# Optimization experiments

Hardware: AMD Instinct MI355X
Metric: run time of the kernel (lower is better)

The kernel has to match this reference:

```python
import jax, jax.numpy as jnp
import numpy as np

N_NODES = 50000
N_EDGES = 800000
H_DIM = 128
HIDDEN = 256


def _glorot(key, shape):
    fan_in, fan_out = shape[1], shape[0]
    lim = np.sqrt(6.0 / (fan_in + fan_out)).astype(np.float32)
    return jax.random.uniform(key, shape, jnp.float32, -lim, lim)


def setup_inputs() -> dict:
    key = jax.random.key(0)
    ks = jax.random.split(key, 12)
    h = jax.random.normal(ks[0], (N_NODES, H_DIM), jnp.float32)
    coord_diff = jax.random.normal(ks[1], (N_EDGES, 3), jnp.float32)
    row = jax.random.randint(ks[2], (N_EDGES,), 0, N_NODES, jnp.int64)
    col = jax.random.randint(ks[3], (N_EDGES,), 0, N_NODES, jnp.int64)
    # edge MLP: Linear(2*H+1 -> HIDDEN), SiLU, Linear(HIDDEN -> HIDDEN), SiLU
    We1 = _glorot(ks[4], (HIDDEN, 2 * H_DIM + 1))
    be1 = jnp.zeros((HIDDEN,), jnp.float32)
    We2 = _glorot(ks[5], (HIDDEN, HIDDEN))
    be2 = jnp.zeros((HIDDEN,), jnp.float32)
    # node MLP: Linear(HIDDEN + H -> HIDDEN), SiLU, Linear(HIDDEN -> H)
    Wn1 = _glorot(ks[6], (HIDDEN, HIDDEN + H_DIM))
    bn1 = jnp.zeros((HIDDEN,), jnp.float32)
    Wn2 = _glorot(ks[7], (H_DIM, HIDDEN))
    bn2 = jnp.zeros((H_DIM,), jnp.float32)
    return {"h": h, "coord_diff": coord_diff, "row": row, "col": col,
            "We1": We1, "be1": be1, "We2": We2, "be2": be2,
            "Wn1": Wn1, "bn1": bn1, "Wn2": Wn2, "bn2": bn2}


def reference(h, coord_diff, row, col, We1, be1, We2, be2, Wn1, bn1, Wn2, bn2):
    # radial: squared edge length, [E, 1]
    radial = jnp.sum(coord_diff ** 2, axis=1, keepdims=True)
    # edge model: gather endpoints, concat, 2-layer SiLU MLP
    e_in = jnp.concatenate([h[row], h[col], radial], axis=1)  # [E, 2H+1]
    m = jax.nn.silu(e_in @ We1.T + be1)                        # [E, HIDDEN]
    m = jax.nn.silu(m @ We2.T + be2)                           # [E, HIDDEN]
    # node model: scatter-add messages to source node `row`
    agg = jax.ops.segment_sum(m, row, num_segments=h.shape[0])  # [N, HIDDEN]
    n_in = jnp.concatenate([h, agg], axis=1)                    # [N, HIDDEN+H]
    out = jax.nn.silu(n_in @ Wn1.T + bn1) @ Wn2.T + bn2         # [N, H]
    return out
```

## Files before the change

kernel.cpp:

```cpp
#include <hip/hip_runtime.h>
#include <cstdint>
#include <cstddef>

#define E_EDGES 800000
#define N_NODES 50000
#define HDIM 128
#define HID 256
#define ME 64
#define NB 64
#define NTILES 196

typedef __attribute__((ext_vector_type(8))) short short8;
typedef __attribute__((ext_vector_type(4))) float f32x4;

__device__ __forceinline__ float silu(float y) {
    return y * __builtin_amdgcn_rcpf(1.0f + __expf(-y));
}

__device__ __forceinline__ short f2bfn(float f) {
    __bf16 b = (__bf16)f;
    return __builtin_bit_cast(short, b);
}
__device__ __forceinline__ float bf2f(short s) {
    return __uint_as_float(((unsigned int)(unsigned short)s) << 16);
}

#define PREP_H    6250
#define PREP_AGG  (PREP_H + 12500)
#define PREP_HIST (PREP_AGG + 3125)
#define PREP_WAB  (PREP_HIST + 320)
#define PREP_WRF  (PREP_WAB + 1)
#define PREP_WE2  (PREP_WRF + 288)
#define PREP_WN1  (PREP_WE2 + 416)
#define PREP_WN2  (PREP_WN1 + 144)
__global__ void prep_kernel(const float* __restrict__ h, short* __restrict__ hbf,
                            float* __restrict__ agg,
                            const int* __restrict__ row, int* __restrict__ cnt,
                            const float* __restrict__ We1, const float* __restrict__ be1,
                            short* __restrict__ Wab, float* __restrict__ wrf,
                            const float* __restrict__ We2, const float* __restrict__ be2,
                            short* __restrict__ Wb2,
                            const float* __restrict__ Wn1, const float* __restrict__ bn1,
                            short* __restrict__ Wbn1,
                            const float* __restrict__ Wn2, const float* __restrict__ bn2,
                            short* __restrict__ Wbn2) {
    const int b = blockIdx.x, t = threadIdx.x;
    if (b < PREP_H) {
        int i = b * 256 + t;
        float4 v = ((const float4*)h)[i];
        short4 s;
        s.x = f2bfn(v.x); s.y = f2bfn(v.y); s.z = f2bfn(v.z); s.w = f2bfn(v.w);
        ((short4*)hbf)[i] = s;
    } else if (b < PREP_AGG) {
        int i = (b - PREP_H) * 256 + t;
        ((float4*)agg)[i] = make_float4(0.f, 0.f, 0.f, 0.f);
    } else if (b < PREP_HIST) {
        int e = (b - PREP_AGG) * 256 + t;
        if (e < E_EDGES) atomicAdd(&cnt[row[e]], 1);
    } else if (b < PREP_WAB) {
        int idx = (b - PREP_HIST) * 256 + t;
        int c = idx / 160, k = idx - c * 160;
        short v = 0;
        if (c < 256) {
            if (k < 128)       v = f2bfn(We1[c * 257 + k]);
            else if (k == 128) v = f2bfn(be1[c]);
        } else {
            if (k < 128)       v = f2bfn(We1[(c - 256) * 257 + 128 + k]);
        }
        Wab[idx] = v;
    } else if (b < PREP_WRF) {
        wrf[t] = We1[t * 257 + 256];
    } else if (b < PREP_WE2) {
        int idx = (b - PREP_WRF) * 256 + t;
        int c = idx / 288, k = idx - c * 288;
        short v = 0;
        if (k < 256)       v = f2bfn(We2[c * 256 + k]);
        else if (k == 256) v = f2bfn(be2[c]);
        Wb2[idx] = v;
    } else if (b < PREP_WN1) {
        int idx = (b - PREP_WE2) * 256 + t;
        int c = idx / 416, k = idx - c * 416;
        short v = 0;
        if (k < 384)       v = f2bfn(Wn1[c * 384 + k]);
        else if (k == 384) v = f2bfn(bn1[c]);
        Wbn1[idx] = v;
    } else {
        int idx = (b - PREP_WN1) * 256 + t;
        int c = idx / 288, k = idx - c * 288;
        short v = 0;
        if (k < 256)       v = f2bfn(Wn2[c * 256 + k]);
        else if (k == 256) v = f2bfn(bn2[c]);
        Wbn2[idx] = v;
    }
}

__global__ void scanA_kernel(const int* __restrict__ cnt, int* __restrict__ incl,
                             int* __restrict__ tsum) {
    const int b = blockIdx.x, t = threadIdx.x;
    const int i = b * 256 + t;
    const int lane = t & 63, wv = t >> 6;
    int v = (i < N_NODES) ? cnt[i] : 0;
    int s = v;
#pragma unroll
    for (int off = 1; off < 64; off <<= 1) {
        int u = __shfl_up(s, off, 64);
        if (lane >= off) s += u;
    }
    __shared__ int wsum[4];
    if (lane == 63) wsum[wv] = s;
    __syncthreads();
    int pre = 0;
#pragma unroll
    for (int j = 0; j < 3; ++j) if (wv > j) pre += wsum[j];
    s += pre;
    if (i < N_NODES) incl[i] = s;
    if (t == 255) tsum[b] = s;
}

__global__ void scanB_kernel(const int* __restrict__ tsum, int* __restrict__ toff) {
    const int t = threadIdx.x;
    const int lane = t & 63, wv = t >> 6;
    int v = (t < NTILES) ? tsum[t] : 0;
    int s = v;
#pragma unroll
    for (int off = 1; off < 64; off <<= 1) {
        int u = __shfl_up(s, off, 64);
        if (lane >= off) s += u;
    }
    __shared__ int wsum[4];
    if (lane == 63) wsum[wv] = s;
    __syncthreads();
    int pre = 0;
#pragma unroll
    for (int j = 0; j < 3; ++j) if (wv > j) pre += wsum[j];
    s += pre;
    if (t < NTILES) toff[t] = s - v;
}

__global__ void scanC_kernel(const int* __restrict__ cnt, int* __restrict__ cursor,
                             const int* __restrict__ toff) {
    const int b = blockIdx.x, t = threadIdx.x;
    const int i = b * 256 + t;
    if (i < N_NODES) {
        cursor[i] = cursor[i] - cnt[i] + toff[b];
    }
}

__global__ void fill_kernel(const int* __restrict__ row, int* __restrict__ cursor,
                            int* __restrict__ eidx) {
    int e = blockIdx.x * 256 + threadIdx.x;
    if (e < E_EDGES) {
        int pos = atomicAdd(&cursor[row[e]], 1);
        eidx[pos] = e;
    }
}

__global__ __launch_bounds__(256, 4) void hab_kernel(
    const short* __restrict__ hbf, const short* __restrict__ Wab,
    short* __restrict__ hab)
{
    __shared__ __align__(16) short shH[NB * 128];
    __shared__ __align__(16) short shTh[NB * 32];

    const int t = threadIdx.x;
    const int tile = blockIdx.x >> 1;
    const int half = blockIdx.x & 1;
    const int n0 = tile * NB;

    {
        const int n = t >> 2, q = t & 3;
        int gn = n0 + n;
        if (gn >= N_NODES) gn = N_NODES - 1;
        const short8* hp = (const short8*)(hbf + (size_t)gn * HDIM + q * 32);
#pragma unroll
        for (int c = 0; c < 4; ++c) {
            short8 v = hp[c];
            int chunk = q * 4 + c;
            *(short8*)&shH[n * 128 + ((chunk ^ (n & 7)) << 3)] = v;
        }
        short8 z = {0, 0, 0, 0, 0, 0, 0, 0};
        if (q == 0) z[0] = (short)0x3F80;
        *(short8*)&shTh[n * 32 + ((q ^ (n & 3)) << 3)] = z;
    }
    __syncthreads();

    const int l = t & 63, w = t >> 6;
    const int l15 = l & 15, lq = l >> 4;

    f32x4 acc[4][4];
#pragma unroll
    for (int i = 0; i < 4; ++i)
#pragma unroll
        for (int j = 0; j < 4; ++j) acc[i][j] = (f32x4){0.f, 0.f, 0.f, 0.f};

#pragma unroll
    for (int ks = 0; ks < 5; ++ks) {
        short8 a[4], b[4];
#pragma unroll
        for (int et = 0; et < 4; ++et) {
            int r = et * 16 + l15;
            if (ks < 4) {
                int chunk = ks * 4 + lq;
                a[et] = *(const short8*)&shH[r * 128 + ((chunk ^ (r & 7)) << 3)];
            } else {
                a[et] = *(const short8*)&shTh[r * 32 + ((lq ^ (r & 3)) << 3)];
            }
        }
#pragma unroll
        for (int ct = 0; ct < 4; ++ct) {
            int cc = half * 256 + w * 64 + ct * 16 + l15;
            b[ct] = *(const short8*)&Wab[cc * 160 + ks * 32 + lq * 8];
        }
#pragma unroll
        for (int et = 0; et < 4; ++et)
#pragma unroll
            for (int ct = 0; ct < 4; ++ct)
                acc[et][ct] = __builtin_amdgcn_mfma_f32_16x16x32_bf16(
                    a[et], b[ct], acc[et][ct], 0, 0, 0);
    }

#pragma unroll
    for (int et = 0; et < 4; ++et) {
#pragma unroll
        for (int ct = 0; ct < 4; ++ct) {
            int cc = half * 256 + w * 64 + ct * 16 + l15;
#pragma unroll
            for (int r4 = 0; r4 < 4; ++r4) {
                int gn = n0 + et * 16 + lq * 4 + r4;
                if (gn < N_NODES)
                    hab[(size_t)gn * 512 + cc] = f2bfn(acc[et][ct][r4]);
            }
        }
    }
}

__global__ __launch_bounds__(256, 4) void edge_kernel(
    const short* __restrict__ hab, const float* __restrict__ coord,
    const int* __restrict__ row, const int* __restrict__ col,
    const int* __restrict__ eidx, const float* __restrict__ wrf,
    const short* __restrict__ Wb2, float* __restrict__ agg)
{
    __shared__ __align__(16) short shPool[ME * 256 + ME * 32];
    __shared__ int sr[ME];
    short* shA = shPool;
    short* shT = shPool + ME * 256;

    const int t = threadIdx.x;
    const int nwg = E_EDGES / ME;
    const int qq = nwg >> 3, rr = nwg & 7;
    const int xcd = blockIdx.x & 7, bi = blockIdx.x >> 3;
    const int wg = (xcd < rr ? xcd * (qq + 1) : rr * (qq + 1) + (xcd - rr) * qq) + bi;
    const int e0 = wg * ME;

    {
        const int e = t >> 2, q = t & 3;
        const int eo = eidx[e0 + e];
        const int rsrc = row[eo];
        const int csrc = col[eo];
        float cx = coord[3 * eo + 0];
        float cy = coord[3 * eo + 1];
        float cz = coord[3 * eo + 2];
        float radial = cx * cx + cy * cy + cz * cz;
        const short8* Ap = (const short8*)(hab + (size_t)rsrc * 512 + q * 64);
        const short8* Bp = (const short8*)(hab + (size_t)csrc * 512 + 256 + q * 64);
        const f32x4* Wp = (const f32x4*)(wrf + q * 64);
#pragma unroll
        for (int j = 0; j < 8; ++j) {
            short8 av = Ap[j];
            short8 bv = Bp[j];
            f32x4 w0 = Wp[2 * j], w1 = Wp[2 * j + 1];
            short8 o;
#pragma unroll
            for (int u = 0; u < 4; ++u) {
                float y = bf2f(av[u]) + bf2f(bv[u]) + radial * w0[u];
                o[u] = f2bfn(silu(y));
            }
#pragma unroll
            for (int u = 0; u < 4; ++u) {
                float y = bf2f(av[4 + u]) + bf2f(bv[4 + u]) + radial * w1[u];
                o[4 + u] = f2bfn(silu(y));
            }
            int chunk = q * 8 + j;
            *(short8*)&shA[e * 256 + ((chunk ^ (e & 7)) << 3)] = o;
        }
        short8 z = {0, 0, 0, 0, 0, 0, 0, 0};
        if (q == 0) {
            z[0] = (short)0x3F80;
            sr[e] = rsrc;
        }
        *(short8*)&shT[e * 32 + ((q ^ (e & 3)) << 3)] = z;
    }
    __syncthreads();

    const int l = t & 63, w = t >> 6;
    const int l15 = l & 15, lq = l >> 4;

    f32x4 acc[4][4];
#pragma unroll
    for (int i = 0; i < 4; ++i)
#pragma unroll
        for (int j = 0; j < 4; ++j) acc[i][j] = (f32x4){0.f, 0.f, 0.f, 0.f};
#pragma unroll
    for (int ks = 0; ks < 8; ++ks) {
        short8 a[4], b[4];
#pragma unroll
        for (int et = 0; et < 4; ++et) {
            int r = et * 16 + l15;
            int chunk = ks * 4 + lq;
            a[et] = *(const short8*)&shA[r * 256 + ((chunk ^ (r & 7)) << 3)];
        }
#pragma unroll
        for (int ct = 0; ct < 4; ++ct) {
            int cc = w * 64 + ct * 16 + l15;
            b[ct] = *(const short8*)&Wb2[cc * 288 + ks * 32 + lq * 8];
        }
        __builtin_amdgcn_s_setprio(1);
#pragma unroll
        for (int et = 0; et < 4; ++et)
#pragma unroll
            for (int ct = 0; ct < 4; ++ct)
                acc[et][ct] = __builtin_amdgcn_mfma_f32_16x16x32_bf16(
                    a[et], b[ct], acc[et][ct], 0, 0, 0);
        __builtin_amdgcn_s_setprio(0);
    }
    {
        short8 a[4], b[4];
#pragma unroll
        for (int et = 0; et < 4; ++et) {
            int r = et * 16 + l15;
            a[et] = *(const short8*)&shT[r * 32 + ((lq ^ (r & 3)) << 3)];
        }
#pragma unroll
        for (int ct = 0; ct < 4; ++ct) {
            int cc = w * 64 + ct * 16 + l15;
            b[ct] = *(const short8*)&Wb2[cc * 288 + 256 + lq * 8];
        }
        __builtin_amdgcn_s_setprio(1);
#pragma unroll
        for (int et = 0; et < 4; ++et)
#pragma unroll
            for (int ct = 0; ct < 4; ++ct)
                acc[et][ct] = __builtin_amdgcn_mfma_f32_16x16x32_bf16(
                    a[et], b[ct], acc[et][ct], 0, 0, 0);
        __builtin_amdgcn_s_setprio(0);
    }
    __syncthreads();

    {
#pragma unroll
        for (int ct = 0; ct < 4; ++ct) {
#pragma unroll
            for (int et = 0; et < 4; ++et) {
                int kc = w * 64 + ct * 16 + l15;
                int er0 = et * 16 + lq * 4;
                short4 s;
                s.x = f2bfn(silu(acc[et][ct][0]));
                s.y = f2bfn(silu(acc[et][ct][1]));
                s.z = f2bfn(silu(acc[et][ct][2]));
                s.w = f2bfn(silu(acc[et][ct][3]));
                *(short4*)&shPool[kc * 68 + er0] = s;
            }
        }
    }
    __syncthreads();

    {
        const int cc = t;
        const short* myrow = &shPool[cc * 68];
        float accum = 0.f;
        int cur = __builtin_amdgcn_readfirstlane(sr[0]);
        for (int eb = 0; eb < ME; eb += 4) {
            short4 v4 = *(const short4*)&myrow[eb];
            short vj[4] = {v4.x, v4.y, v4.z, v4.w};
#pragma unroll
            for (int j = 0; j < 4; ++j) {
                float v = bf2f(vj[j]);
                int r = __builtin_amdgcn_readfirstlane(sr[eb + j]);
                if (r != cur) {
                    atomicAdd(&agg[(size_t)cur * HID + cc], accum);
                    accum = v;
                    cur = r;
                } else {
                    accum += v;
                }
            }
        }
        atomicAdd(&agg[(size_t)cur * HID + cc], accum);
    }
}

__global__ __launch_bounds__(256, 3) void node_kernel(
    const short* __restrict__ hbf, const float* __restrict__ agg,
    const short* __restrict__ Wbn1, const short* __restrict__ Wbn2,
    float* __restrict__ out)
{
    __shared__ __align__(16) short pool[NB * 384];
    __shared__ __align__(16) short shTn[NB * 32];
    short* shH  = pool;
    short* shAg = pool + NB * 128;
    short* shM  = pool;

    const int t  = threadIdx.x;
    const int n0 = blockIdx.x * NB;

    {
        const int n = t >> 2, q = t & 3;
        int gn = n0 + n;
        if (gn >= N_NODES) gn = N_NODES - 1;
        const short8* hp = (const short8*)(hbf + (size_t)gn * HDIM + q * 32);
#pragma unroll
        for (int c = 0; c < 4; ++c) {
            short8 v = hp[c];
            int chunk = q * 4 + c;
            int sw = chunk ^ (n & 7);
            *(short8*)&shH[n * 128 + sw * 8] = v;
        }
        const float4* ap = (const float4*)(agg + (size_t)gn * HID + q * 64);
#pragma unroll
        for (int i = 0; i < 8; ++i) {
            float4 u0 = ap[2 * i], u1 = ap[2 * i + 1];
            short8 s;
            s[0] = f2bfn(u0.x); s[1] = f2bfn(u0.y); s[2] = f2bfn(u0.z); s[3] = f2bfn(u0.w);
            s[4] = f2bfn(u1.x); s[5] = f2bfn(u1.y); s[6] = f2bfn(u1.z); s[7] = f2bfn(u1.w);
            int chunk = q * 8 + i;
            int sw2 = chunk ^ (n & 7);
            *(short8*)&shAg[n * 256 + sw2 * 8] = s;
        }
        short8 z = {0, 0, 0, 0, 0, 0, 0, 0};
        if (q == 0) z[0] = (short)0x3F80;
        *(short8*)&shTn[n * 32 + ((q ^ (n & 3)) << 3)] = z;
    }
    __syncthreads();

    const int l = t & 63, w = t >> 6;
    const int l15 = l & 15, lq = l >> 4;

    f32x4 acc[4][4];
#pragma unroll
    for (int i = 0; i < 4; ++i)
#pragma unroll
        for (int j = 0; j < 4; ++j) acc[i][j] = (f32x4){0.f, 0.f, 0.f, 0.f};
#pragma unroll
    for (int ks = 0; ks < 12; ++ks) {
        short8 a[4], b[4];
#pragma unroll
        for (int et = 0; et < 4; ++et) {
            int r = et * 16 + l15;
            if (ks < 4) {
                int chunk = ks * 4 + lq;
                a[et] = *(const short8*)&shH[r * 128 + ((chunk ^ (r & 7)) << 3)];
            } else {
                int chunk = (ks - 4) * 4 + lq;
                a[et] = *(const short8*)&shAg[r * 256 + ((chunk ^ (r & 7)) << 3)];
            }
        }
#pragma unroll
        for (int ct = 0; ct < 4; ++ct) {
            int cc = w * 64 + ct * 16 + l15;
            b[ct] = *(const short8*)&Wbn1[cc * 416 + ks * 32 + lq * 8];
        }
#pragma unroll
        for (int et = 0; et < 4; ++et)
#pragma unroll
            for (int ct = 0; ct < 4; ++ct)
                acc[et][ct] = __builtin_amdgcn_mfma_f32_16x16x32_bf16(
                    a[et], b[ct], acc[et][ct], 0, 0, 0);
    }
    {
        short8 a[4], b[4];
#pragma unroll
        for (int et = 0; et < 4; ++et) {
            int r = et * 16 + l15;
            a[et] = *(const short8*)&shTn[r * 32 + ((lq ^ (r & 3)) << 3)];
        }
#pragma unroll
        for (int ct = 0; ct < 4; ++ct) {
            int cc = w * 64 + ct * 16 + l15;
            b[ct] = *(const short8*)&Wbn1[cc * 416 + 384 + lq * 8];
        }
#pragma unroll
        for (int et = 0; et < 4; ++et)
#pragma unroll
            for (int ct = 0; ct < 4; ++ct)
                acc[et][ct] = __builtin_amdgcn_mfma_f32_16x16x32_bf16(
                    a[et], b[ct], acc[et][ct], 0, 0, 0);
    }
    __syncthreads();

    {
#pragma unroll
        for (int et = 0; et < 4; ++et) {
#pragma unroll
            for (int rp = 0; rp < 2; ++rp) {
                int er0 = et * 16 + lq * 4 + rp * 2;
#pragma unroll
                for (int ct = 0; ct < 4; ++ct) {
                    int kc = w * 64 + ct * 16 + l15;
                    float y0 = silu(acc[et][ct][rp * 2]);
                    float y1 = silu(acc[et][ct][rp * 2 + 1]);
                    int khi = kc >> 3, klo = kc & 7;
                    shM[er0 * 256 + ((khi ^ (er0 & 7)) << 3) + klo] = f2bfn(y0);
                    shM[(er0 + 1) * 256 + ((khi ^ ((er0 + 1) & 7)) << 3) + klo] = f2bfn(y1);
                }
            }
        }
    }
    __syncthreads();

    f32x4 acc2[4][2];
#pragma unroll
    for (int i = 0; i < 4; ++i)
#pragma unroll
        for (int j = 0; j < 2; ++j) acc2[i][j] = (f32x4){0.f, 0.f, 0.f, 0.f};
#pragma unroll
    for (int ks = 0; ks < 8; ++ks) {
        short8 a[4], b2[2];
#pragma unroll
        for (int et = 0; et < 4; ++et) {
            int r = et * 16 + l15;
            int chunk = ks * 4 + lq;
            a[et] = *(const short8*)&shM[r * 256 + ((chunk ^ (r & 7)) << 3)];
        }
#pragma unroll
        for (int ct = 0; ct < 2; ++ct) {
            int cc = w * 32 + ct * 16 + l15;
            b2[ct] = *(const short8*)&Wbn2[cc * 288 + ks * 32 + lq * 8];
        }
#pragma unroll
        for (int et = 0; et < 4; ++et)
#pragma unroll
            for (int ct = 0; ct < 2; ++ct)
                acc2[et][ct] = __builtin_amdgcn_mfma_f32_16x16x32_bf16(
                    a[et], b2[ct], acc2[et][ct], 0, 0, 0);
    }
    {
        short8 a[4], b2[2];
#pragma unroll
        for (int et = 0; et < 4; ++et) {
            int r = et * 16 + l15;
            a[et] = *(const short8*)&shTn[r * 32 + ((lq ^ (r & 3)) << 3)];
        }
#pragma unroll
        for (int ct = 0; ct < 2; ++ct) {
            int cc = w * 32 + ct * 16 + l15;
            b2[ct] = *(const short8*)&Wbn2[cc * 288 + 256 + lq * 8];
        }
#pragma unroll
        for (int et = 0; et < 4; ++et)
#pragma unroll
            for (int ct = 0; ct < 2; ++ct)
                acc2[et][ct] = __builtin_amdgcn_mfma_f32_16x16x32_bf16(
                    a[et], b2[ct], acc2[et][ct], 0, 0, 0);
    }

#pragma unroll
    for (int et = 0; et < 4; ++et) {
#pragma unroll
        for (int ct = 0; ct < 2; ++ct) {
            int cc = w * 32 + ct * 16 + l15;
#pragma unroll
            for (int r4 = 0; r4 < 4; ++r4) {
                int gn = n0 + et * 16 + lq * 4 + r4;
                if (gn < N_NODES)
                    out[(size_t)gn * HDIM + cc] = acc2[et][ct][r4];
            }
        }
    }
}

extern "C" void kernel_launch(void* const* d_in, const int* in_sizes, int n_in,
                              void* d_out, int out_size, void* d_ws, size_t ws_size,
                              hipStream_t stream) {
    const float* h   = (const float*)d_in[0];
    const float* cd  = (const float*)d_in[1];
    const int*   row = (const int*)d_in[2];
    const int*   col = (const int*)d_in[3];
    const float* We1 = (const float*)d_in[4];
    const float* be1 = (const float*)d_in[5];
    const float* We2 = (const float*)d_in[6];
    const float* be2 = (const float*)d_in[7];
    const float* Wn1 = (const float*)d_in[8];
    const float* bn1 = (const float*)d_in[9];
    const float* Wn2 = (const float*)d_in[10];
    const float* bn2 = (const float*)d_in[11];
    float* out = (float*)d_out;

    short* Wab  = (short*)d_ws;
    short* Wb2  = Wab + 512 * 160;
    short* Wbn1 = Wb2 + 256 * 288;
    short* Wbn2 = Wbn1 + 256 * 416;
    float* wrf  = (float*)(Wbn2 + 128 * 288);
    short* hbf  = (short*)(wrf + 256);
    short* hab  = hbf + (size_t)N_NODES * HDIM;
    float* agg  = (float*)(hab + (size_t)N_NODES * 512);
    int*   cnt    = (int*)(agg + (size_t)N_NODES * HID);
    int*   cursor = cnt + N_NODES;
    int*   eidx   = cursor + N_NODES;
    int*   tsum   = eidx + E_EDGES;
    int*   toff   = tsum + 256;

    hipMemsetAsync(cnt, 0, N_NODES * sizeof(int), stream);

    prep_kernel<<<PREP_WN2, 256, 0, stream>>>(h, hbf, agg, row, cnt,
                                              We1, be1, Wab, wrf,
                                              We2, be2, Wb2,
                                              Wn1, bn1, Wbn1, Wn2, bn2, Wbn2);

    hab_kernel<<<((N_NODES + NB - 1) / NB) * 2, 256, 0, stream>>>(hbf, Wab, hab);

    scanA_kernel<<<NTILES, 256, 0, stream>>>(cnt, cursor, tsum);
    scanB_kernel<<<1, 256, 0, stream>>>(tsum, toff);
    scanC_kernel<<<NTILES, 256, 0, stream>>>(cnt, cursor, toff);
    fill_kernel<<<(E_EDGES + 255) / 256, 256, 0, stream>>>(row, cursor, eidx);

    edge_kernel<<<E_EDGES / ME, 256, 0, stream>>>(hab, cd, row, col, eidx, wrf,
                                                  Wb2, agg);
    node_kernel<<<(N_NODES + NB - 1) / NB, 256, 0, stream>>>(hbf, agg, Wbn1, Wbn2, out);
}
```

Measured before the change: 492.4 us.

## Gather endpoint features into LDS with async global_load_lds in edge kernel

The edge kernel's gather of the row and column endpoint feature rows now goes straight into shared memory through asynchronous global-to-LDS 16-byte loads. Each wave broadcasts row and column indices by shuffle and lays the data out with an XOR swizzle. The SiLU pre-activation then reads both halves from LDS, with radial values and radial weights staged in shared memory, and writes results in place. The aim is to cut register traffic and improve latency hiding on the random gathers. In exchange LDS use roughly doubles, so launch bounds drop from 4 to 2 blocks per CU, which lowers occupancy.

```diff
diff --git a/kernel.cpp b/kernel.cpp
--- a/kernel.cpp
+++ b/kernel.cpp
@@ -23,6 +23,12 @@
 }
 __device__ __forceinline__ float bf2f(short s) {
     return __uint_as_float(((unsigned int)(unsigned short)s) << 16);
+}
+
+__device__ __forceinline__ void async16(void* lds, const void* g) {
+    __builtin_amdgcn_global_load_lds(
+        (const __attribute__((address_space(1))) unsigned int*)g,
+        (__attribute__((address_space(3))) unsigned int*)lds, 16, 0, 0);
 }
 
 #define PREP_H    6250
@@ -234,16 +240,17 @@
     }
 }
 
-__global__ __launch_bounds__(256, 4) void edge_kernel(
+__global__ __launch_bounds__(256, 2) void edge_kernel(
     const short* __restrict__ hab, const float* __restrict__ coord,
     const int* __restrict__ row, const int* __restrict__ col,
     const int* __restrict__ eidx, const float* __restrict__ wrf,
     const short* __restrict__ Wb2, float* __restrict__ agg)
 {
-    __shared__ __align__(16) short shPool[ME * 256 + ME * 32];
-    __shared__ int sr[ME];
-    short* shA = shPool;
-    short* shT = shPool + ME * 256;
+    __shared__ __align__(16) short shPool[ME * 512];
+    __shared__ __align__(16) short shT[ME * 32];
+    __shared__ int   sr[ME];
+    __shared__ float srad[ME];
+    __shared__ __align__(16) float shWr[HID];
 
     const int t = threadIdx.x;
     const int nwg = E_EDGES / ME;
@@ -252,48 +259,71 @@
     const int wg = (xcd < rr ? xcd * (qq + 1) : rr * (qq + 1) + (xcd - rr) * qq) + bi;
     const int e0 = wg * ME;
 
-    {
-        const int e = t >> 2, q = t & 3;
-        const int eo = eidx[e0 + e];
-        const int rsrc = row[eo];
-        const int csrc = col[eo];
+    const int l = t & 63, w = t >> 6;
+
+    int m_r = 0, m_c = 0;
+    if (l < 16) {
+        int e = 16 * w + l;
+        int eo = eidx[e0 + e];
+        m_r = row[eo];
+        m_c = col[eo];
         float cx = coord[3 * eo + 0];
         float cy = coord[3 * eo + 1];
         float cz = coord[3 * eo + 2];
-        float radial = cx * cx + cy * cy + cz * cz;
-        const short8* Ap = (const short8*)(hab + (size_t)rsrc * 512 + q * 64);
-        const short8* Bp = (const short8*)(hab + (size_t)csrc * 512 + 256 + q * 64);
-        const f32x4* Wp = (const f32x4*)(wrf + q * 64);
+        sr[e]   = m_r;
+        srad[e] = cx * cx + cy * cy + cz * cz;
+    }
+    if (w == 0) {
+        ((float4*)shWr)[l] = ((const float4*)wrf)[l];
+    }
+
+    {
+        char* ldsA = (char*)shPool + (size_t)w * 8192;
+        char* ldsB = (char*)shPool + 32768 + (size_t)w * 8192;
+        const int half = l >> 5;
+        const int c32  = l & 31;
+#pragma unroll
+        for (int i = 0; i < 8; ++i) {
+            int sel = 2 * i + half;
+            int rs  = __shfl(m_r, sel, 64);
+            int cs  = __shfl(m_c, sel, 64);
+            int ch  = c32 ^ (sel & 7);
+            async16(ldsA + i * 1024, hab + (size_t)rs * 512 + ch * 8);
+            async16(ldsB + i * 1024, hab + (size_t)cs * 512 + 256 + ch * 8);
+        }
+    }
+    __syncthreads();
+
+    {
+        const int e = t >> 2, q = t & 3;
+        const float radial = srad[e];
+        short* rowA = shPool + e * 256;
+        const short* rowB = shPool + 16384 + e * 256;
 #pragma unroll
         for (int j = 0; j < 8; ++j) {
-            short8 av = Ap[j];
-            short8 bv = Bp[j];
-            f32x4 w0 = Wp[2 * j], w1 = Wp[2 * j + 1];
+            int s  = 8 * q + ((j + e) & 7);
+            int ch = s ^ (e & 7);
+            short8 a = *(const short8*)&rowA[s * 8];
+            short8 b = *(const short8*)&rowB[s * 8];
+            f32x4 w0 = *(const f32x4*)&shWr[ch * 8];
+            f32x4 w1 = *(const f32x4*)&shWr[ch * 8 + 4];
             short8 o;
 #pragma unroll
-            for (int u = 0; u < 4; ++u) {
-                float y = bf2f(av[u]) + bf2f(bv[u]) + radial * w0[u];
-                o[u] = f2bfn(silu(y));
-            }
-#pragma unroll
-            for (int u = 0; u < 4; ++u) {
-                float y = bf2f(av[4 + u]) + bf2f(bv[4 + u]) + radial * w1[u];
-                o[4 + u] = f2bfn(silu(y));
-            }
-            int chunk = q * 8 + j;
-            *(short8*)&shA[e * 256 + ((chunk ^ (e & 7)) << 3)] = o;
+            for (int u = 0; u < 4; ++u)
+                o[u] = f2bfn(silu(bf2f(a[u]) + bf2f(b[u]) + radial * w0[u]));
+#pragma unroll
+            for (int u = 0; u < 4; ++u)
+                o[4 + u] = f2bfn(silu(bf2f(a[4 + u]) + bf2f(b[4 + u]) + radial * w1[u]));
+            *(short8*)&rowA[s * 8] = o;
         }
         short8 z = {0, 0, 0, 0, 0, 0, 0, 0};
-        if (q == 0) {
-            z[0] = (short)0x3F80;
-            sr[e] = rsrc;
-        }
+        if (q == 0) z[0] = (short)0x3F80;
         *(short8*)&shT[e * 32 + ((q ^ (e & 3)) << 3)] = z;
     }
     __syncthreads();
 
-    const int l = t & 63, w = t >> 6;
     const int l15 = l & 15, lq = l >> 4;
+    short* shA = shPool;
 
     f32x4 acc[4][4];
 #pragma unroll
```

New measurement: 527.1 us. 1.07x slower.
